# Kernel tuning notes

Hardware: AMD Instinct MI355X
Metric: run time of the kernel (lower is better)

The kernel has to match this reference:

```python
import jax, jax.numpy as jnp
import numpy as np

N_NODES = 100_000
N_EDGES = 1_600_000
HIDDEN = 64
EPS = 1e-5  # eqx.nn.RMSNorm default eps


def setup_inputs() -> dict:
    key = jax.random.key(0)
    k1, k2, k3 = jax.random.split(key, 3)
    x = jax.random.normal(k1, (N_NODES, HIDDEN), dtype=jnp.float32)
    # edges[0] = target node i, edges[1] = source node j  (a[i, j] = 1 => edge j -> i)
    edges = jax.random.randint(k2, (2, N_EDGES), 0, N_NODES, dtype=jnp.int32)
    W = jax.random.normal(k3, (HIDDEN, HIDDEN), dtype=jnp.float32) * (1.0 / np.sqrt(HIDDEN))
    b = jnp.zeros((HIDDEN,), dtype=jnp.float32)
    norm_weight = jnp.ones((HIDDEN,), dtype=jnp.float32)
    norm_bias = jnp.zeros((HIDDEN,), dtype=jnp.float32)
    return {"x": x, "edges": edges, "W": W, "b": b,
            "norm_weight": norm_weight, "norm_bias": norm_bias}


def reference(x, edges, W, b, norm_weight, norm_bias):
    n_nodes = x.shape[0]
    # vmap(Linear) + relu:  m = relu(x @ W.T + b)
    m = jax.nn.relu(jnp.einsum('nd,kd->nk', x, W) + b)
    # a @ m : sum-aggregate messages from source j into target i
    dst, src = edges[0], edges[1]
    agg = jax.ops.segment_sum(m[src], dst, num_segments=n_nodes)
    # residual + RMSNorm (per-node)
    h = x + agg
    inv_rms = jax.lax.rsqrt(jnp.mean(h * h, axis=-1, keepdims=True) + EPS)
    return norm_weight * (h * inv_rms) + norm_bias
```

## Files before the change

kernel.cpp:

```cpp
#include <hip/hip_runtime.h>
#include <hip/hip_bf16.h>

#define N_NODES 100000
#define N_EDGES 1600000
#define HID 64

#define NG 192
#define GROUPS 521
#define GSTRIDE 544
#define NREP 2
#define RCAP 2048
#define EPT 16
#define BIN_BLOCKS 391
#define LIN_BLOCKS 1563

#define TILES 12
#define TCAP 384
#define GTHREADS 768
#define GWAVES 12
#define PADTAG (16 << 17)

using bf16 = __hip_bfloat16;
typedef __attribute__((ext_vector_type(8))) short short8;
typedef __attribute__((ext_vector_type(4))) short short4v;
typedef __attribute__((ext_vector_type(4))) float float4v;

__device__ __forceinline__ float bfbits2f(unsigned short u) {
    union { unsigned int i; float f; } v;
    v.i = ((unsigned int)u) << 16;
    return v.f;
}
__device__ __forceinline__ unsigned short f2bfbits(float f) {
    union { float f; unsigned int i; } v;
    v.f = f;
    unsigned int r = v.i + 0x7fffu + ((v.i >> 16) & 1u);
    return (unsigned short)(r >> 16);
}

__global__ __launch_bounds__(256) void k_init(
    const float* __restrict__ W, int* __restrict__ gcur,
    unsigned short* __restrict__ Wfhi, unsigned short* __restrict__ Wflo)
{
    const int t = blockIdx.x * 256 + threadIdx.x;
    for (int i = t; i < NREP * GSTRIDE; i += 512) gcur[i] = 0;
    for (int o = t; o < HID * HID; o += 512) {
        const int j = o & 7, l = (o >> 3) & 63, ksnt = o >> 9;
        const int ks = ksnt & 1, nt = ksnt >> 1;
        const int c = l & 15, q = l >> 4;
        const float f = W[(size_t)(nt * 16 + c) * HID + ks * 32 + q * 8 + j];
        const unsigned short h = f2bfbits(f);
        Wfhi[o] = h;
        Wflo[o] = f2bfbits(f - bfbits2f(h));
    }
}

__global__ __launch_bounds__(256, 4) void k_prep2(
    const float* __restrict__ x, const unsigned short* __restrict__ Wfhi,
    const unsigned short* __restrict__ Wflo, const float* __restrict__ b,
    bf16* __restrict__ m,
    const int* __restrict__ edges, int* __restrict__ gcur,
    int* __restrict__ binned)
{
    __shared__ union SM {
        struct { float xs[64 * 65]; } lin;
        struct { int cnt[GSTRIDE]; int base[GSTRIDE]; } bin;
    } sm;
    const int t = threadIdx.x;

    if (blockIdx.x < LIN_BLOCKS) {
        const int nb0 = blockIdx.x * 64;
        const float4* xg = reinterpret_cast<const float4*>(x) + (size_t)nb0 * 16;
        #pragma unroll
        for (int k = 0; k < 4; ++k) {
            const int f4 = t + k * 256;
            float4 v = make_float4(0.f, 0.f, 0.f, 0.f);
            if (nb0 * 16 + f4 < N_NODES * 16) v = xg[f4];
            const int r = f4 >> 4, fc = (f4 & 15) * 4;
            float* dst = &sm.lin.xs[r * 65 + fc];
            dst[0] = v.x; dst[1] = v.y; dst[2] = v.z; dst[3] = v.w;
        }
        __syncthreads();

        const int wv = t >> 6, l = t & 63;
        const int c = l & 15, q = l >> 4;
        const int tile = blockIdx.x * 4 + wv;
        if (tile >= N_NODES / 16) return;
        const int nb = tile * 16;

        const short8* wfh = reinterpret_cast<const short8*>(Wfhi);
        const short8* wfl = reinterpret_cast<const short8*>(Wflo);
        short8 Bhi[4][2], Blo[4][2];
        #pragma unroll
        for (int nt = 0; nt < 4; ++nt)
            #pragma unroll
            for (int ks = 0; ks < 2; ++ks) {
                const int fi = (nt * 2 + ks) * 64 + l;
                Bhi[nt][ks] = wfh[fi];
                Blo[nt][ks] = wfl[fi];
            }

        short8 Ahi[2];
        #pragma unroll
        for (int ks = 0; ks < 2; ++ks) {
            const float* xsrc = &sm.lin.xs[(wv * 16 + c) * 65 + ks * 32 + q * 8];
            #pragma unroll
            for (int j = 0; j < 8; ++j)
                Ahi[ks][j] = (short)f2bfbits(xsrc[j]);
        }

        float4v acc[4];
        #pragma unroll
        for (int nt = 0; nt < 4; ++nt) {
            const float bias = b[nt * 16 + c];
            acc[nt] = (float4v){bias, bias, bias, bias};
            #pragma unroll
            for (int ks = 0; ks < 2; ++ks) {
                acc[nt] = __builtin_amdgcn_mfma_f32_16x16x32_bf16(Ahi[ks], Bhi[nt][ks], acc[nt], 0, 0, 0);
                acc[nt] = __builtin_amdgcn_mfma_f32_16x16x32_bf16(Ahi[ks], Blo[nt][ks], acc[nt], 0, 0, 0);
            }
        }

        unsigned short* mp = reinterpret_cast<unsigned short*>(m);
        #pragma unroll
        for (int nt = 0; nt < 4; ++nt)
            #pragma unroll
            for (int rg = 0; rg < 4; ++rg) {
                const float v = fmaxf(acc[nt][rg], 0.0f);
                mp[(size_t)(nb + q * 4 + rg) * HID + nt * 16 + c] = f2bfbits(v);
            }
    } else {
        int* cnt  = sm.bin.cnt;
        int* base = sm.bin.base;
        const int bb = blockIdx.x - LIN_BLOCKS;
        for (int i = t; i < GSTRIDE; i += 256) cnt[i] = 0;
        __syncthreads();

        const int e0 = bb * (256 * EPT);
        int gk[EPT], pk[EPT], sl[EPT];
        #pragma unroll
        for (int k = 0; k < EPT; ++k) {
            const int e = e0 + k * 256 + t;
            if (e < N_EDGES) {
                const int dst = edges[e];
                const int src = edges[N_EDGES + e];
                const int g = (int)((unsigned)dst / NG);
                gk[k] = g;
                pk[k] = ((dst - g * NG) << 17) | src;
                sl[k] = atomicAdd(&cnt[g], 1);
            } else gk[k] = -1;
        }
        __syncthreads();
        const int r = bb & (NREP - 1);
        for (int i = t; i < GROUPS; i += 256) {
            const int cc = cnt[i];
            base[i] = cc ? atomicAdd(&gcur[r * GSTRIDE + i], cc) : 0;
        }
        __syncthreads();
        #pragma unroll
        for (int k = 0; k < EPT; ++k) {
            if (gk[k] >= 0) {
                const int pos = base[gk[k]] + sl[k];
                if ((unsigned)pos < RCAP)
                    binned[(size_t)(r * GSTRIDE + gk[k]) * RCAP + pos] = pk[k];
            }
        }
    }
}

#define TRREAD(dst, OFF) \
    asm volatile("ds_read_b64_tr_b16 %0, %1 offset:" #OFF \
                 : "=v"(dst) : "v"(traddr) : "memory")

__global__ __launch_bounds__(GTHREADS, 6) void k_gather_mfma(
    const float* __restrict__ x, const bf16* __restrict__ m,
    const int* __restrict__ gcur, const int* __restrict__ binned,
    const float* __restrict__ nw, const float* __restrict__ nbias,
    float* __restrict__ out)
{
    __shared__ int tcnt[TILES];
    __shared__ int tlist[TILES * TCAP];
    __shared__ uint4 stg4[GWAVES * 128];

    const int t = threadIdx.x;
    const int g = blockIdx.x;
    if (t < TILES) tcnt[t] = 0;
    __syncthreads();

    #pragma unroll
    for (int rr = 0; rr < NREP; ++rr) {
        int c = gcur[rr * GSTRIDE + g];
        if (c > RCAP) c = RCAP;
        const int* reg = binned + (size_t)(rr * GSTRIDE + g) * RCAP;
        for (int i = t; i < c; i += GTHREADS) {
            const int pr = reg[i];
            const int tile = pr >> 21;
            const int slot = atomicAdd(&tcnt[tile], 1);
            if (slot < TCAP) tlist[tile * TCAP + slot] = pr & 0x1FFFFF;
        }
    }
    __syncthreads();

    const int wv = t >> 6, l = t & 63;
    const int q = l >> 4;
    const int node16 = l & 15;
    const int h  = l & 1;
    const int r2 = (l >> 1) & 3;
    const int ft = (l >> 3) & 3;
    const int qb = (l >> 5) & 1;
    const int fq = ft * 2 + h;
    const int sA0 = qb * 8 + r2 * 2;
    const int wbyte = ft * 512 + qb * 128 + r2 * 32 + h * 16;
    char* stg_wave = (char*)(&stg4[0]) + (wv << 11);
    const unsigned traddr = (unsigned)(size_t)stg_wave + (unsigned)(l << 3);
    const uint4* mv = reinterpret_cast<const uint4*>(m);

    const int tile = wv;
    int K = tcnt[tile];
    if (K > TCAP) K = TCAP;
    const int lbase = tile * TCAP;
    const int nch = (K + 31) >> 5;

    for (int i = K + l; i < nch * 32; i += 64) tlist[lbase + i] = PADTAG;

    float4v acc0 = {0.f, 0.f, 0.f, 0.f};
    float4v acc1 = acc0, acc2 = acc0, acc3 = acc0;

    if (nch > 0) {
        int2 pa = *reinterpret_cast<const int2*>(&tlist[lbase + sA0]);
        int2 pb = *reinterpret_cast<const int2*>(&tlist[lbase + sA0 + 16]);
        uint4 dA0 = mv[(size_t)(pa.x & 0x1FFFF) * 8 + fq];
        uint4 dA1 = mv[(size_t)(pb.x & 0x1FFFF) * 8 + fq];
        uint4 dB0 = mv[(size_t)(pa.y & 0x1FFFF) * 8 + fq];
        uint4 dB1 = mv[(size_t)(pb.y & 0x1FFFF) * 8 + fq];

        for (int ch = 0; ch < nch; ++ch) {
            const int k0 = ch << 5;
            const int kn = (ch + 1 < nch) ? (k0 + 32) : 0;
            const int2 npa = *reinterpret_cast<const int2*>(&tlist[lbase + kn + sA0]);
            const int2 npb = *reinterpret_cast<const int2*>(&tlist[lbase + kn + sA0 + 16]);
            const uint4 nA0 = mv[(size_t)(npa.x & 0x1FFFF) * 8 + fq];
            const uint4 nA1 = mv[(size_t)(npb.x & 0x1FFFF) * 8 + fq];
            const uint4 nB0 = mv[(size_t)(npa.y & 0x1FFFF) * 8 + fq];
            const uint4 nB1 = mv[(size_t)(npb.y & 0x1FFFF) * 8 + fq];

            const int4 t0 = *reinterpret_cast<const int4*>(&tlist[lbase + k0 + q * 8]);
            const int4 t1 = *reinterpret_cast<const int4*>(&tlist[lbase + k0 + q * 8 + 4]);
            short8 bh;
            bh[0] = (short)(((t0.x >> 17) == node16) ? 0x3F80 : 0);
            bh[4] = (short)(((t0.y >> 17) == node16) ? 0x3F80 : 0);
            bh[1] = (short)(((t0.z >> 17) == node16) ? 0x3F80 : 0);
            bh[5] = (short)(((t0.w >> 17) == node16) ? 0x3F80 : 0);
            bh[2] = (short)(((t1.x >> 17) == node16) ? 0x3F80 : 0);
            bh[6] = (short)(((t1.y >> 17) == node16) ? 0x3F80 : 0);
            bh[3] = (short)(((t1.z >> 17) == node16) ? 0x3F80 : 0);
            bh[7] = (short)(((t1.w >> 17) == node16) ? 0x3F80 : 0);

            *reinterpret_cast<uint4*>(stg_wave + wbyte) = dA0;
            *reinterpret_cast<uint4*>(stg_wave + wbyte + 256) = dA1;
            short4v tA0, tA1, tA2, tA3;
            TRREAD(tA0, 0); TRREAD(tA1, 512); TRREAD(tA2, 1024); TRREAD(tA3, 1536);

            *reinterpret_cast<uint4*>(stg_wave + wbyte) = dB0;
            *reinterpret_cast<uint4*>(stg_wave + wbyte + 256) = dB1;
            short4v tB0, tB1, tB2, tB3;
            TRREAD(tB0, 0); TRREAD(tB1, 512); TRREAD(tB2, 1024); TRREAD(tB3, 1536);

            asm volatile("s_waitcnt lgkmcnt(0)" ::: "memory");
            __builtin_amdgcn_sched_barrier(0);
            const short8 a0 = __builtin_shufflevector(tA0, tB0, 0, 1, 2, 3, 4, 5, 6, 7);
            const short8 a1 = __builtin_shufflevector(tA1, tB1, 0, 1, 2, 3, 4, 5, 6, 7);
            const short8 a2 = __builtin_shufflevector(tA2, tB2, 0, 1, 2, 3, 4, 5, 6, 7);
            const short8 a3 = __builtin_shufflevector(tA3, tB3, 0, 1, 2, 3, 4, 5, 6, 7);
            acc0 = __builtin_amdgcn_mfma_f32_16x16x32_bf16(a0, bh, acc0, 0, 0, 0);
            acc1 = __builtin_amdgcn_mfma_f32_16x16x32_bf16(a1, bh, acc1, 0, 0, 0);
            acc2 = __builtin_amdgcn_mfma_f32_16x16x32_bf16(a2, bh, acc2, 0, 0, 0);
            acc3 = __builtin_amdgcn_mfma_f32_16x16x32_bf16(a3, bh, acc3, 0, 0, 0);

            pa = npa; pb = npb;
            dA0 = nA0; dA1 = nA1; dB0 = nB0; dB1 = nB1;
        }
    }

    const int dl = (tile << 4) + node16;
    const int n = g * NG + dl;
    if (n < N_NODES) {
        const float4* xr = reinterpret_cast<const float4*>(x) + (size_t)n * 16 + q;
        const float4 x0 = xr[0], x1 = xr[4], x2 = xr[8], x3 = xr[12];
        const float h00 = x0.x + acc0[0], h01 = x0.y + acc0[1], h02 = x0.z + acc0[2], h03 = x0.w + acc0[3];
        const float h10 = x1.x + acc1[0], h11 = x1.y + acc1[1], h12 = x1.z + acc1[2], h13 = x1.w + acc1[3];
        const float h20 = x2.x + acc2[0], h21 = x2.y + acc2[1], h22 = x2.z + acc2[2], h23 = x2.w + acc2[3];
        const float h30 = x3.x + acc3[0], h31 = x3.y + acc3[1], h32 = x3.z + acc3[2], h33 = x3.w + acc3[3];
        float ss = h00 * h00 + h01 * h01 + h02 * h02 + h03 * h03
                 + h10 * h10 + h11 * h11 + h12 * h12 + h13 * h13
                 + h20 * h20 + h21 * h21 + h22 * h22 + h23 * h23
                 + h30 * h30 + h31 * h31 + h32 * h32 + h33 * h33;
        ss += __shfl_xor(ss, 16, 64);
        ss += __shfl_xor(ss, 32, 64);
        const float inv = rsqrtf(ss * (1.0f / HID) + 1e-5f);
        const float4* nwp = reinterpret_cast<const float4*>(nw);
        const float4* nbp = reinterpret_cast<const float4*>(nbias);
        float4* op = reinterpret_cast<float4*>(out) + (size_t)n * 16 + q;
        {
            const float4 w = nwp[q], bb = nbp[q];
            float4 o;
            o.x = w.x * h00 * inv + bb.x; o.y = w.y * h01 * inv + bb.y;
            o.z = w.z * h02 * inv + bb.z; o.w = w.w * h03 * inv + bb.w;
            op[0] = o;
        }
        {
            const float4 w = nwp[4 + q], bb = nbp[4 + q];
            float4 o;
            o.x = w.x * h10 * inv + bb.x; o.y = w.y * h11 * inv + bb.y;
            o.z = w.z * h12 * inv + bb.z; o.w = w.w * h13 * inv + bb.w;
            op[4] = o;
        }
        {
            const float4 w = nwp[8 + q], bb = nbp[8 + q];
            float4 o;
            o.x = w.x * h20 * inv + bb.x; o.y = w.y * h21 * inv + bb.y;
            o.z = w.z * h22 * inv + bb.z; o.w = w.w * h23 * inv + bb.w;
            op[8] = o;
        }
        {
            const float4 w = nwp[12 + q], bb = nbp[12 + q];
            float4 o;
            o.x = w.x * h30 * inv + bb.x; o.y = w.y * h31 * inv + bb.y;
            o.z = w.z * h32 * inv + bb.z; o.w = w.w * h33 * inv + bb.w;
            op[12] = o;
        }
    }
}

extern "C" void kernel_launch(void* const* d_in, const int* in_sizes, int n_in,
                              void* d_out, int out_size, void* d_ws, size_t ws_size,
                              hipStream_t stream) {
    const float* x     = (const float*)d_in[0];
    const int*   edges = (const int*)d_in[1];
    const float* W     = (const float*)d_in[2];
    const float* b     = (const float*)d_in[3];
    const float* nw    = (const float*)d_in[4];
    const float* nb    = (const float*)d_in[5];
    float* out = (float*)d_out;

    int* gcur = (int*)d_ws;
    unsigned short* Wfhi = (unsigned short*)((char*)d_ws + (1 << 14));
    unsigned short* Wflo = Wfhi + HID * HID;
    int*  binned = (int*)((char*)d_ws + (1 << 16));
    bf16* m      = (bf16*)((char*)d_ws + (1 << 16) +
                           (size_t)NREP * GSTRIDE * RCAP * sizeof(int));

    k_init<<<2, 256, 0, stream>>>(W, gcur, Wfhi, Wflo);
    k_prep2<<<LIN_BLOCKS + BIN_BLOCKS, 256, 0, stream>>>(x, Wfhi, Wflo, b, m, edges, gcur, binned);
    k_gather_mfma<<<GROUPS, GTHREADS, 0, stream>>>(x, m, gcur, binned, nw, nb, out);
}
```

Baseline: 150.6 us.

## Bin edges directly into per-tile global lists, dropping two-level group binning

The binning kernel now does one global atomicAdd per edge, keyed on the 16-node destination tile, and writes straight into per-tile lists in global memory. This removes the shared-memory group histogram, the per-group global reservation and the second LDS re-bin stage in the gather kernel. The gather kernel maps one wave per tile, reads its list straight from global memory and masks the tail entries instead of padding them. The trade is far more global atomics (1.6M, heavily contended) in exchange for removing a sync-heavy intermediate stage.

```diff
diff --git a/kernel.cpp b/kernel.cpp
--- a/kernel.cpp
+++ b/kernel.cpp
@@ -5,20 +5,13 @@
 #define N_EDGES 1600000
 #define HID 64
 
-#define NG 192
-#define GROUPS 521
-#define GSTRIDE 544
-#define NREP 2
-#define RCAP 2048
+#define NTILES 6250
+#define TCAP 384
 #define EPT 16
 #define BIN_BLOCKS 391
 #define LIN_BLOCKS 1563
-
-#define TILES 12
-#define TCAP 384
-#define GTHREADS 768
-#define GWAVES 12
-#define PADTAG (16 << 17)
+#define GWAVES 8
+#define GBLOCKS 782
 
 using bf16 = __hip_bfloat16;
 typedef __attribute__((ext_vector_type(8))) short short8;
@@ -42,7 +35,7 @@
     unsigned short* __restrict__ Wfhi, unsigned short* __restrict__ Wflo)
 {
     const int t = blockIdx.x * 256 + threadIdx.x;
-    for (int i = t; i < NREP * GSTRIDE; i += 512) gcur[i] = 0;
+    for (int i = t; i < 6272; i += 512) gcur[i] = 0;
     for (int o = t; o < HID * HID; o += 512) {
         const int j = o & 7, l = (o >> 3) & 63, ksnt = o >> 9;
         const int ks = ksnt & 1, nt = ksnt >> 1;
@@ -61,10 +54,7 @@
     const int* __restrict__ edges, int* __restrict__ gcur,
     int* __restrict__ binned)
 {
-    __shared__ union SM {
-        struct { float xs[64 * 65]; } lin;
-        struct { int cnt[GSTRIDE]; int base[GSTRIDE]; } bin;
-    } sm;
+    __shared__ float xs[64 * 65];
     const int t = threadIdx.x;
 
     if (blockIdx.x < LIN_BLOCKS) {
@@ -76,7 +66,7 @@
             float4 v = make_float4(0.f, 0.f, 0.f, 0.f);
             if (nb0 * 16 + f4 < N_NODES * 16) v = xg[f4];
             const int r = f4 >> 4, fc = (f4 & 15) * 4;
-            float* dst = &sm.lin.xs[r * 65 + fc];
+            float* dst = &xs[r * 65 + fc];
             dst[0] = v.x; dst[1] = v.y; dst[2] = v.z; dst[3] = v.w;
         }
         __syncthreads();
@@ -84,7 +74,7 @@
         const int wv = t >> 6, l = t & 63;
         const int c = l & 15, q = l >> 4;
         const int tile = blockIdx.x * 4 + wv;
-        if (tile >= N_NODES / 16) return;
+        if (tile >= NTILES) return;
         const int nb = tile * 16;
 
         const short8* wfh = reinterpret_cast<const short8*>(Wfhi);
@@ -102,7 +92,7 @@
         short8 Ahi[2];
         #pragma unroll
         for (int ks = 0; ks < 2; ++ks) {
-            const float* xsrc = &sm.lin.xs[(wv * 16 + c) * 65 + ks * 32 + q * 8];
+            const float* xsrc = &xs[(wv * 16 + c) * 65 + ks * 32 + q * 8];
             #pragma unroll
             for (int j = 0; j < 8; ++j)
                 Ahi[ks][j] = (short)f2bfbits(xsrc[j]);
@@ -129,39 +119,18 @@
                 mp[(size_t)(nb + q * 4 + rg) * HID + nt * 16 + c] = f2bfbits(v);
             }
     } else {
-        int* cnt  = sm.bin.cnt;
-        int* base = sm.bin.base;
         const int bb = blockIdx.x - LIN_BLOCKS;
-        for (int i = t; i < GSTRIDE; i += 256) cnt[i] = 0;
-        __syncthreads();
-
         const int e0 = bb * (256 * EPT);
-        int gk[EPT], pk[EPT], sl[EPT];
         #pragma unroll
         for (int k = 0; k < EPT; ++k) {
             const int e = e0 + k * 256 + t;
             if (e < N_EDGES) {
                 const int dst = edges[e];
                 const int src = edges[N_EDGES + e];
-                const int g = (int)((unsigned)dst / NG);
-                gk[k] = g;
-                pk[k] = ((dst - g * NG) << 17) | src;
-                sl[k] = atomicAdd(&cnt[g], 1);
-            } else gk[k] = -1;
-        }
-        __syncthreads();
-        const int r = bb & (NREP - 1);
-        for (int i = t; i < GROUPS; i += 256) {
-            const int cc = cnt[i];
-            base[i] = cc ? atomicAdd(&gcur[r * GSTRIDE + i], cc) : 0;
-        }
-        __syncthreads();
-        #pragma unroll
-        for (int k = 0; k < EPT; ++k) {
-            if (gk[k] >= 0) {
-                const int pos = base[gk[k]] + sl[k];
-                if ((unsigned)pos < RCAP)
-                    binned[(size_t)(r * GSTRIDE + gk[k]) * RCAP + pos] = pk[k];
+                const int tile = dst >> 4;
+                const int slot = atomicAdd(&gcur[tile], 1);
+                if (slot < TCAP)
+                    binned[(size_t)tile * TCAP + slot] = ((dst & 15) << 17) | src;
             }
         }
     }
@@ -171,36 +140,18 @@
     asm volatile("ds_read_b64_tr_b16 %0, %1 offset:" #OFF \
                  : "=v"(dst) : "v"(traddr) : "memory")
 
-__global__ __launch_bounds__(GTHREADS, 6) void k_gather_mfma(
+__global__ __launch_bounds__(512, 8) void k_gather_mfma(
     const float* __restrict__ x, const bf16* __restrict__ m,
     const int* __restrict__ gcur, const int* __restrict__ binned,
     const float* __restrict__ nw, const float* __restrict__ nbias,
     float* __restrict__ out)
 {
-    __shared__ int tcnt[TILES];
-    __shared__ int tlist[TILES * TCAP];
     __shared__ uint4 stg4[GWAVES * 128];
-
     const int t = threadIdx.x;
-    const int g = blockIdx.x;
-    if (t < TILES) tcnt[t] = 0;
-    __syncthreads();
-
-    #pragma unroll
-    for (int rr = 0; rr < NREP; ++rr) {
-        int c = gcur[rr * GSTRIDE + g];
-        if (c > RCAP) c = RCAP;
-        const int* reg = binned + (size_t)(rr * GSTRIDE + g) * RCAP;
-        for (int i = t; i < c; i += GTHREADS) {
-            const int pr = reg[i];
-            const int tile = pr >> 21;
-            const int slot = atomicAdd(&tcnt[tile], 1);
-            if (slot < TCAP) tlist[tile * TCAP + slot] = pr & 0x1FFFFF;
-        }
-    }
-    __syncthreads();
-
     const int wv = t >> 6, l = t & 63;
+    const int tg = blockIdx.x * GWAVES + wv;
+    if (tg >= NTILES) return;
+
     const int q = l >> 4;
     const int node16 = l & 15;
     const int h  = l & 1;
@@ -214,46 +165,46 @@
     const unsigned traddr = (unsigned)(size_t)stg_wave + (unsigned)(l << 3);
     const uint4* mv = reinterpret_cast<const uint4*>(m);
 
-    const int tile = wv;
-    int K = tcnt[tile];
+    int K = gcur[tg];
     if (K > TCAP) K = TCAP;
-    const int lbase = tile * TCAP;
+    const int* list = binned + (size_t)tg * TCAP;
     const int nch = (K + 31) >> 5;
-
-    for (int i = K + l; i < nch * 32; i += 64) tlist[lbase + i] = PADTAG;
 
     float4v acc0 = {0.f, 0.f, 0.f, 0.f};
     float4v acc1 = acc0, acc2 = acc0, acc3 = acc0;
 
     if (nch > 0) {
-        int2 pa = *reinterpret_cast<const int2*>(&tlist[lbase + sA0]);
-        int2 pb = *reinterpret_cast<const int2*>(&tlist[lbase + sA0 + 16]);
+        const int ka = sA0, kb2 = sA0 + 16;
+        int2 pa = *reinterpret_cast<const int2*>(list + ((ka  < K) ? ka  : 0));
+        int2 pb = *reinterpret_cast<const int2*>(list + ((kb2 < K) ? kb2 : 0));
         uint4 dA0 = mv[(size_t)(pa.x & 0x1FFFF) * 8 + fq];
+        uint4 dB0 = mv[(size_t)(pa.y & 0x1FFFF) * 8 + fq];
         uint4 dA1 = mv[(size_t)(pb.x & 0x1FFFF) * 8 + fq];
-        uint4 dB0 = mv[(size_t)(pa.y & 0x1FFFF) * 8 + fq];
         uint4 dB1 = mv[(size_t)(pb.y & 0x1FFFF) * 8 + fq];
 
         for (int ch = 0; ch < nch; ++ch) {
             const int k0 = ch << 5;
             const int kn = (ch + 1 < nch) ? (k0 + 32) : 0;
-            const int2 npa = *reinterpret_cast<const int2*>(&tlist[lbase + kn + sA0]);
-            const int2 npb = *reinterpret_cast<const int2*>(&tlist[lbase + kn + sA0 + 16]);
+            const int na = kn + sA0, nb2 = kn + sA0 + 16;
+            const int2 npa = *reinterpret_cast<const int2*>(list + ((na  < K) ? na  : 0));
+            const int2 npb = *reinterpret_cast<const int2*>(list + ((nb2 < K) ? nb2 : 0));
             const uint4 nA0 = mv[(size_t)(npa.x & 0x1FFFF) * 8 + fq];
+            const uint4 nB0 = mv[(size_t)(npa.y & 0x1FFFF) * 8 + fq];
             const uint4 nA1 = mv[(size_t)(npb.x & 0x1FFFF) * 8 + fq];
-            const uint4 nB0 = mv[(size_t)(npa.y & 0x1FFFF) * 8 + fq];
             const uint4 nB1 = mv[(size_t)(npb.y & 0x1FFFF) * 8 + fq];
 
-            const int4 t0 = *reinterpret_cast<const int4*>(&tlist[lbase + k0 + q * 8]);
-            const int4 t1 = *reinterpret_cast<const int4*>(&tlist[lbase + k0 + q * 8 + 4]);
+            const int tb = k0 + q * 8;
+            const int4 t0 = *reinterpret_cast<const int4*>(list + tb);
+            const int4 t1 = *reinterpret_cast<const int4*>(list + tb + 4);
             short8 bh;
-            bh[0] = (short)(((t0.x >> 17) == node16) ? 0x3F80 : 0);
-            bh[4] = (short)(((t0.y >> 17) == node16) ? 0x3F80 : 0);
-            bh[1] = (short)(((t0.z >> 17) == node16) ? 0x3F80 : 0);
-            bh[5] = (short)(((t0.w >> 17) == node16) ? 0x3F80 : 0);
-            bh[2] = (short)(((t1.x >> 17) == node16) ? 0x3F80 : 0);
-            bh[6] = (short)(((t1.y >> 17) == node16) ? 0x3F80 : 0);
-            bh[3] = (short)(((t1.z >> 17) == node16) ? 0x3F80 : 0);
-            bh[7] = (short)(((t1.w >> 17) == node16) ? 0x3F80 : 0);
+            bh[0] = (short)(((tb + 0 < K) && ((t0.x >> 17) == node16)) ? 0x3F80 : 0);
+            bh[4] = (short)(((tb + 1 < K) && ((t0.y >> 17) == node16)) ? 0x3F80 : 0);
+            bh[1] = (short)(((tb + 2 < K) && ((t0.z >> 17) == node16)) ? 0x3F80 : 0);
+            bh[5] = (short)(((tb + 3 < K) && ((t0.w >> 17) == node16)) ? 0x3F80 : 0);
+            bh[2] = (short)(((tb + 4 < K) && ((t1.x >> 17) == node16)) ? 0x3F80 : 0);
+            bh[6] = (short)(((tb + 5 < K) && ((t1.y >> 17) == node16)) ? 0x3F80 : 0);
+            bh[3] = (short)(((tb + 6 < K) && ((t1.z >> 17) == node16)) ? 0x3F80 : 0);
+            bh[7] = (short)(((tb + 7 < K) && ((t1.w >> 17) == node16)) ? 0x3F80 : 0);
 
             *reinterpret_cast<uint4*>(stg_wave + wbyte) = dA0;
             *reinterpret_cast<uint4*>(stg_wave + wbyte + 256) = dA1;
@@ -277,13 +228,12 @@
             acc3 = __builtin_amdgcn_mfma_f32_16x16x32_bf16(a3, bh, acc3, 0, 0, 0);
 
             pa = npa; pb = npb;
-            dA0 = nA0; dA1 = nA1; dB0 = nB0; dB1 = nB1;
+            dA0 = nA0; dB0 = nB0; dA1 = nA1; dB1 = nB1;
         }
     }
 
-    const int dl = (tile << 4) + node16;
-    const int n = g * NG + dl;
-    if (n < N_NODES) {
+    const int n = tg * 16 + node16;
+    {
         const float4* xr = reinterpret_cast<const float4*>(x) + (size_t)n * 16 + q;
         const float4 x0 = xr[0], x1 = xr[4], x2 = xr[8], x3 = xr[12];
         const float h00 = x0.x + acc0[0], h01 = x0.y + acc0[1], h02 = x0.z + acc0[2], h03 = x0.w + acc0[3];
@@ -343,13 +293,13 @@
     float* out = (float*)d_out;
 
     int* gcur = (int*)d_ws;
-    unsigned short* Wfhi = (unsigned short*)((char*)d_ws + (1 << 14));
+    unsigned short* Wfhi = (unsigned short*)((char*)d_ws + (1 << 15));
     unsigned short* Wflo = Wfhi + HID * HID;
     int*  binned = (int*)((char*)d_ws + (1 << 16));
     bf16* m      = (bf16*)((char*)d_ws + (1 << 16) +
-                           (size_t)NREP * GSTRIDE * RCAP * sizeof(int));
+                           (size_t)(NTILES + 1) * TCAP * sizeof(int));
 
     k_init<<<2, 256, 0, stream>>>(W, gcur, Wfhi, Wflo);
     k_prep2<<<LIN_BLOCKS + BIN_BLOCKS, 256, 0, stream>>>(x, Wfhi, Wflo, b, m, edges, gcur, binned);
-    k_gather_mfma<<<GROUPS, GTHREADS, 0, stream>>>(x, m, gcur, binned, nw, nb, out);
-}
+    k_gather_mfma<<<GBLOCKS, 512, 0, stream>>>(x, m, gcur, binned, nw, nb, out);
+}
```

Result: slower. 249.6 us (+65.7%).
